# Kernel tuning notes

Hardware: AMD Instinct MI355X
Metric: run time of the kernel (lower is better)

## Reference

```python
import jax, jax.numpy as jnp
import numpy as np

GROUP_SIZE = 128  # per-group absmax scaling along the feature dim
ALPHA = 1.0       # group_size > 0 branch forces alpha = 1.0
# 4-bit signed non-uniform 'flint' grid (e2m1-style), sorted ascending, 15 levels
GRID_VALUES = np.array([-6.0, -4.0, -3.0, -2.0, -1.5, -1.0, -0.5, 0.0,
                        0.5, 1.0, 1.5, 2.0, 3.0, 4.0, 6.0], dtype=np.float32)


def quantize_with_grid(x, grid, group_size, alpha):
    """Group-wise fake quantization: scale each group by alpha*absmax/max|grid|,
    snap to nearest grid value, dequantize. Matches ANT quantize_with_grid."""
    orig_shape = x.shape
    xg = x.reshape(-1, group_size)                       # [G, group_size]
    gmax = jnp.max(jnp.abs(grid))
    maxv = jnp.max(jnp.abs(xg), axis=1, keepdims=True) * alpha
    scale = maxv / gmax                                  # [G, 1]
    scale = jnp.where(scale == 0, jnp.float32(1.0), scale)
    xs = xg / scale
    # nearest-grid lookup via midpoints + searchsorted (memory-light, exact)
    mid = (grid[1:] + grid[:-1]) * 0.5                   # [K-1]
    idx = jnp.searchsorted(mid, xs)                      # [G, group_size]
    q = jnp.take(grid, idx)
    return (q * scale).reshape(orig_shape)


def setup_inputs() -> dict:
    key = jax.random.key(0)
    k1, k2, k3 = jax.random.split(key, 3)
    x = jax.random.normal(k1, (4, 4096, 4096), dtype=jnp.float32)
    # weight buffer is the already-dequantized (calibrated) weight
    weight = jax.random.normal(k2, (1024, 4096), dtype=jnp.float32) * 0.02
    bias = jax.random.normal(k3, (1024,), dtype=jnp.float32) * 0.01
    grid = jnp.asarray(GRID_VALUES)
    return {"x": x, "weight": weight, "bias": bias, "grid": grid}


def reference(x, weight, bias, grid):
    # ANT_Linear.forward, calibrated steady state:
    #   input_2d = x.reshape(-1, in_features)
    #   deq_input = quantize_with_grid(input_2d, grid, group_size, alpha=1.0)
    #   out = F.linear(deq_input, weight) + bias
    out_shape = x.shape[:-1] + (weight.shape[0],)
    x2d = x.reshape(-1, x.shape[-1])                     # [N, in_features]
    deq = quantize_with_grid(x2d, grid, GROUP_SIZE, ALPHA)
    out = jnp.einsum('ni,oi->no', deq, weight) + bias    # [N, out_features]
    return out.reshape(out_shape)
```

## Files before the change

### kernel.cpp

```cpp
#include <hip/hip_runtime.h>
#include <hip/hip_bf16.h>

using bf16x8 = __attribute__((ext_vector_type(8))) __bf16;
using f32x4  = __attribute__((ext_vector_type(4))) float;
typedef unsigned short ushort_t;

#define M_DIM 16384
#define K_DIM 4096
#define N_DIM 1024

#define BARR() __builtin_amdgcn_s_barrier()

__device__ __forceinline__ unsigned short f2bf(float f) {
  __hip_bfloat16 h = __float2bfloat16(f);
  return *reinterpret_cast<unsigned short*>(&h);
}

__device__ __forceinline__ float snap(float a) {
  float q = 0.0f;
  q += (a > 0.25f) ? 0.5f : 0.0f;
  q += (a > 0.75f) ? 0.5f : 0.0f;
  q += (a > 1.25f) ? 0.5f : 0.0f;
  q += (a > 1.75f) ? 0.5f : 0.0f;
  q += (a > 2.5f)  ? 1.0f : 0.0f;
  q += (a > 3.5f)  ? 1.0f : 0.0f;
  q += (a > 5.0f)  ? 2.0f : 0.0f;
  return q;
}

__device__ __forceinline__ unsigned short qdq(float xv, float rs, float scale) {
  float xs = xv * rs;
  float q  = copysignf(snap(fabsf(xs)), xs);
  return f2bf(q * scale);
}

__global__ __launch_bounds__(256) void quant_kernel(const float* __restrict__ x,
                                                    unsigned short* __restrict__ dq) {
  const int wid = (blockIdx.x << 2) + (threadIdx.x >> 6);
  const int l   = threadIdx.x & 63;
  const int sub = l >> 4, t = l & 15;
  const size_t base = ((size_t)wid * 4 + sub) * 128;
  const float4* px = reinterpret_cast<const float4*>(x + base);
  float4 v0 = px[t];
  float4 v1 = px[16 + t];
  float amax = fmaxf(fmaxf(fmaxf(fabsf(v0.x), fabsf(v0.y)), fmaxf(fabsf(v0.z), fabsf(v0.w))),
                     fmaxf(fmaxf(fabsf(v1.x), fabsf(v1.y)), fmaxf(fabsf(v1.z), fabsf(v1.w))));
  #pragma unroll
  for (int m = 1; m < 16; m <<= 1) amax = fmaxf(amax, __shfl_xor(amax, m, 64));
  float scale = amax / 6.0f;
  if (scale == 0.0f) scale = 1.0f;
  const float rs = 1.0f / scale;
  ushort4 o0, o1;
  o0.x = qdq(v0.x, rs, scale); o0.y = qdq(v0.y, rs, scale);
  o0.z = qdq(v0.z, rs, scale); o0.w = qdq(v0.w, rs, scale);
  o1.x = qdq(v1.x, rs, scale); o1.y = qdq(v1.y, rs, scale);
  o1.z = qdq(v1.z, rs, scale); o1.w = qdq(v1.w, rs, scale);
  reinterpret_cast<ushort4*>(dq + base)[t]      = o0;
  reinterpret_cast<ushort4*>(dq + base)[16 + t] = o1;
}

__global__ __launch_bounds__(256) void wconv_kernel(const float* __restrict__ w,
                                                    unsigned short* __restrict__ o) {
  const int n4 = (N_DIM * K_DIM) / 4;
  for (int i = blockIdx.x * 256 + threadIdx.x; i < n4; i += gridDim.x * 256) {
    float4 v = reinterpret_cast<const float4*>(w)[i];
    ushort4 u;
    u.x = f2bf(v.x); u.y = f2bf(v.y); u.z = f2bf(v.z); u.w = f2bf(v.w);
    reinterpret_cast<ushort4*>(o)[i] = u;
  }
}

__device__ __forceinline__ bf16x8 lds_ld(const ushort_t* p) {
  return *reinterpret_cast<const bf16x8*>(p);
}

template<int OFF>
__device__ __forceinline__ void stg2(ushort_t (&sL)[65536], int wid,
                                     const ushort_t* g0, const ushort_t* g1) {
  __builtin_amdgcn_global_load_lds((const __attribute__((address_space(1))) void*)g0,
      (__attribute__((address_space(3))) void*)(&sL[OFF + wid * 512]), 16, 0, 0);
  __builtin_amdgcn_global_load_lds((const __attribute__((address_space(1))) void*)g1,
      (__attribute__((address_space(3))) void*)(&sL[OFF + 4096 + wid * 512]), 16, 0, 0);
}

template<int P, bool S12, bool S34, int VM>
__device__ __forceinline__ void tile_iter(
    int t, ushort_t (&sL)[65536], int wid, int rab, int rbb,
    const int (&roA)[8], const int (&roB)[4], int swz0, int swz1,
    const ushort_t* pa0, const ushort_t* pa1,
    const ushort_t* pb0, const ushort_t* pb1,
    f32x4 (&acc)[8][4]) {
  constexpr int RP  = P * 32768;
  constexpr int DB1 = (1 - P) * 32768 + 24576;
  constexpr int DA1 = (1 - P) * 32768 + 8192;
  constexpr int DB0 = P * 32768 + 16384;
  constexpr int DA0 = P * 32768;
  bf16x8 aL0[4], aL1[4], aH0[4], aH1[4], b0[4], b1[4];

  #pragma unroll
  for (int i = 0; i < 4; ++i) {
    aL0[i] = lds_ld(&sL[RP + rab + roA[i] + swz0]);
    aL1[i] = lds_ld(&sL[RP + rab + roA[i] + swz1]);
  }
  #pragma unroll
  for (int n = 0; n < 2; ++n) {
    b0[n] = lds_ld(&sL[RP + rbb + roB[n] + swz0]);
    b1[n] = lds_ld(&sL[RP + rbb + roB[n] + swz1]);
  }

  #pragma unroll
  for (int n = 2; n < 4; ++n) {
    b0[n] = lds_ld(&sL[RP + rbb + roB[n] + swz0]);
    b1[n] = lds_ld(&sL[RP + rbb + roB[n] + swz1]);
  }
  if constexpr (S12)
    stg2<DB1>(sL, wid, pb0 + (size_t)128 * K_DIM + (size_t)(t + 1) * 64,
                       pb1 + (size_t)128 * K_DIM + (size_t)(t + 1) * 64);
  __builtin_amdgcn_s_setprio(1);
  #pragma unroll
  for (int i = 0; i < 4; ++i)
    #pragma unroll
    for (int n = 0; n < 2; ++n) {
      acc[i][n] = __builtin_amdgcn_mfma_f32_16x16x32_bf16(aL0[i], b0[n], acc[i][n], 0, 0, 0);
      acc[i][n] = __builtin_amdgcn_mfma_f32_16x16x32_bf16(aL1[i], b1[n], acc[i][n], 0, 0, 0);
    }
  __builtin_amdgcn_s_setprio(0);
  BARR();

  #pragma unroll
  for (int i = 0; i < 4; ++i) {
    aH0[i] = lds_ld(&sL[RP + rab + roA[4 + i] + swz0]);
    aH1[i] = lds_ld(&sL[RP + rab + roA[4 + i] + swz1]);
  }
  if constexpr (S12)
    stg2<DA1>(sL, wid, pa0 + (size_t)128 * K_DIM + (size_t)(t + 1) * 64,
                       pa1 + (size_t)128 * K_DIM + (size_t)(t + 1) * 64);
  __builtin_amdgcn_s_setprio(1);
  #pragma unroll
  for (int i = 0; i < 4; ++i)
    #pragma unroll
    for (int n = 2; n < 4; ++n) {
      acc[i][n] = __builtin_amdgcn_mfma_f32_16x16x32_bf16(aL0[i], b0[n], acc[i][n], 0, 0, 0);
      acc[i][n] = __builtin_amdgcn_mfma_f32_16x16x32_bf16(aL1[i], b1[n], acc[i][n], 0, 0, 0);
    }
  __builtin_amdgcn_s_setprio(0);
  BARR();

  if constexpr (S34)
    stg2<DB0>(sL, wid, pb0 + (size_t)(t + 2) * 64, pb1 + (size_t)(t + 2) * 64);
  __builtin_amdgcn_s_setprio(1);
  #pragma unroll
  for (int i = 0; i < 4; ++i)
    #pragma unroll
    for (int n = 2; n < 4; ++n) {
      acc[4 + i][n] = __builtin_amdgcn_mfma_f32_16x16x32_bf16(aH0[i], b0[n], acc[4 + i][n], 0, 0, 0);
      acc[4 + i][n] = __builtin_amdgcn_mfma_f32_16x16x32_bf16(aH1[i], b1[n], acc[4 + i][n], 0, 0, 0);
    }
  __builtin_amdgcn_s_setprio(0);
  BARR();

  if constexpr (S34)
    stg2<DA0>(sL, wid, pa0 + (size_t)(t + 2) * 64, pa1 + (size_t)(t + 2) * 64);
  __builtin_amdgcn_s_setprio(1);
  #pragma unroll
  for (int i = 0; i < 4; ++i)
    #pragma unroll
    for (int n = 0; n < 2; ++n) {
      acc[4 + i][n] = __builtin_amdgcn_mfma_f32_16x16x32_bf16(aH0[i], b0[n], acc[4 + i][n], 0, 0, 0);
      acc[4 + i][n] = __builtin_amdgcn_mfma_f32_16x16x32_bf16(aH1[i], b1[n], acc[4 + i][n], 0, 0, 0);
    }
  __builtin_amdgcn_s_setprio(0);
  if constexpr (VM == 4) {
    asm volatile("s_waitcnt vmcnt(4)");
    __builtin_amdgcn_sched_barrier(0);
  } else if constexpr (VM == 0) {
    asm volatile("s_waitcnt vmcnt(0)");
    __builtin_amdgcn_sched_barrier(0);
  }
  BARR();
}

__global__ __launch_bounds__(512, 2) void gemm256(const ushort_t* __restrict__ A,
                                                  const ushort_t* __restrict__ B,
                                                  const float* __restrict__ bias,
                                                  float* __restrict__ C) {
  __shared__ ushort_t sL[65536];
  const int tid  = threadIdx.x;
  const int wid  = tid >> 6, lane = tid & 63;
  const int r    = lane & 15, h = lane >> 4;
  const int wm   = wid >> 2, wn = wid & 3;

  const int bid = blockIdx.x;
  const int xcd = bid & 7, j = bid >> 3;
  const int bm  = xcd * 8 + (j >> 2);
  const int bn  = j & 3;

  const int x7   = lane & 7;
  const int swz0 = ((h) ^ x7) << 3;
  const int swz1 = ((4 | h) ^ x7) << 3;
  int roA[8], roB[4];
  #pragma unroll
  for (int m = 0; m < 8; ++m) roA[m] = (m * 16 + r) * 64;
  #pragma unroll
  for (int n = 0; n < 4; ++n) roB[n] = ((wn & 1) * 64 + n * 16 + r) * 64;
  const int rab = wm * 8192;
  const int rbb = 16384 + (wn >> 1) * 8192;

  const int srow0 = tid >> 3;
  const int cst   = ((tid & 7) ^ (srow0 & 7)) << 3;
  const ushort_t* pa0 = A + (size_t)(bm * 256 + srow0) * K_DIM + cst;
  const ushort_t* pa1 = A + (size_t)(bm * 256 + 64 + srow0) * K_DIM + cst;
  const ushort_t* pb0 = B + (size_t)(bn * 256 + srow0) * K_DIM + cst;
  const ushort_t* pb1 = B + (size_t)(bn * 256 + 64 + srow0) * K_DIM + cst;

  f32x4 acc[8][4];
  #pragma unroll
  for (int m = 0; m < 8; ++m)
    #pragma unroll
    for (int n = 0; n < 4; ++n) acc[m][n] = (f32x4){0.f, 0.f, 0.f, 0.f};

  stg2<16384>(sL, wid, pb0, pb1);
  stg2<0>    (sL, wid, pa0, pa1);
  stg2<24576>(sL, wid, pb0 + (size_t)128 * K_DIM, pb1 + (size_t)128 * K_DIM);
  stg2<8192> (sL, wid, pa0 + (size_t)128 * K_DIM, pa1 + (size_t)128 * K_DIM);
  stg2<49152>(sL, wid, pb0 + 64, pb1 + 64);
  stg2<32768>(sL, wid, pa0 + 64, pa1 + 64);
  asm volatile("s_waitcnt vmcnt(4)");
  __builtin_amdgcn_sched_barrier(0);
  BARR();

  for (int t = 0; t < 62; t += 2) {
    tile_iter<0, true, true, 4>(t,     sL, wid, rab, rbb, roA, roB, swz0, swz1,
                                pa0, pa1, pb0, pb1, acc);
    tile_iter<1, true, true, 4>(t + 1, sL, wid, rab, rbb, roA, roB, swz0, swz1,
                                pa0, pa1, pb0, pb1, acc);
  }
  tile_iter<0, true, false, 0>(62, sL, wid, rab, rbb, roA, roB, swz0, swz1,
                               pa0, pa1, pb0, pb1, acc);
  tile_iter<1, false, false, -1>(63, sL, wid, rab, rbb, roA, roB, swz0, swz1,
                                 pa0, pa1, pb0, pb1, acc);

  const int orow = bm * 256 + wm * 128;
  const int ocol = bn * 256 + wn * 64;
  #pragma unroll
  for (int n = 0; n < 4; ++n) {
    const int col = ocol + n * 16 + r;
    const float bv = bias[col];
    #pragma unroll
    for (int m = 0; m < 8; ++m) {
      const int rb = orow + m * 16 + h * 4;
      #pragma unroll
      for (int j2 = 0; j2 < 4; ++j2)
        C[(size_t)(rb + j2) * N_DIM + col] = acc[m][n][j2] + bv;
    }
  }
}

__global__ __launch_bounds__(256) void fused_naive(const float* __restrict__ x,
                                                   const float* __restrict__ w,
                                                   const float* __restrict__ bias,
                                                   float* __restrict__ out) {
  __shared__ float xq[K_DIM];
  const int row = blockIdx.x;
  const float* xr = x + (size_t)row * K_DIM;
  const int t = threadIdx.x;
  const int g = t >> 3, s = t & 7;
  float vals[16];
  float amax = 0.f;
  #pragma unroll
  for (int i = 0; i < 16; ++i) {
    vals[i] = xr[g * 128 + s * 16 + i];
    amax = fmaxf(amax, fabsf(vals[i]));
  }
  #pragma unroll
  for (int m = 1; m < 8; m <<= 1) amax = fmaxf(amax, __shfl_xor(amax, m, 64));
  float scale = amax / 6.0f;
  if (scale == 0.f) scale = 1.f;
  const float rs = 1.0f / scale;
  #pragma unroll
  for (int i = 0; i < 16; ++i) {
    float xs = vals[i] * rs;
    xq[g * 128 + s * 16 + i] = copysignf(snap(fabsf(xs)), xs) * scale;
  }
  __syncthreads();
  #pragma unroll
  for (int i = 0; i < 4; ++i) {
    const int o = i * 256 + t;
    const float* wrow = w + (size_t)o * K_DIM;
    float acc = 0.f;
    for (int k = 0; k < K_DIM; k += 4) {
      float4 wv = *reinterpret_cast<const float4*>(wrow + k);
      acc += xq[k] * wv.x + xq[k + 1] * wv.y + xq[k + 2] * wv.z + xq[k + 3] * wv.w;
    }
    out[(size_t)row * N_DIM + o] = acc + bias[o];
  }
}

extern "C" void kernel_launch(void* const* d_in, const int* in_sizes, int n_in,
                              void* d_out, int out_size, void* d_ws, size_t ws_size,
                              hipStream_t stream) {
  const float* x    = (const float*)d_in[0];
  const float* wgt  = (const float*)d_in[1];
  const float* bias = (const float*)d_in[2];
  float* out = (float*)d_out;

  const size_t deq_bytes = (size_t)M_DIM * K_DIM * 2;
  const size_t wb_bytes  = (size_t)N_DIM * K_DIM * 2;
  if (ws_size >= deq_bytes + wb_bytes) {
    ushort_t* deq = (ushort_t*)d_ws;
    ushort_t* wb  = (ushort_t*)((char*)d_ws + deq_bytes);
    quant_kernel<<<(M_DIM * (K_DIM / 128)) / 16, 256, 0, stream>>>(x, deq);
    wconv_kernel<<<1024, 256, 0, stream>>>(wgt, wb);
    gemm256<<<(N_DIM / 256) * (M_DIM / 256), 512, 0, stream>>>(deq, wb, bias, out);
  } else {
    fused_naive<<<M_DIM, 256, 0, stream>>>(x, wgt, bias, out);
  }
}
```

Baseline: 191.0 us.

## Prefetch next tile's A-low and B-low LDS fragments across iteration boundary

The loads of the first A half and B half fragments for the next K tile move to the end of the current iteration, and those registers are carried across iterations. The vmcnt wait moves earlier with a tighter count so the next buffer is ready before the prefetch. The goal is to hide LDS read latency at the start of each tile behind the previous tile's MFMAs. In exchange, register pressure rises from the persistent fragments, and the altered wait placement could stall on global loads.

Result: slower. 358.9 us (+88.0%).

```diff
diff --git a/kernel.cpp b/kernel.cpp
--- a/kernel.cpp
+++ b/kernel.cpp
@@ -83,35 +83,27 @@
       (__attribute__((address_space(3))) void*)(&sL[OFF + 4096 + wid * 512]), 16, 0, 0);
 }
 
-template<int P, bool S12, bool S34, int VM>
+template<int P, bool S12, bool S34, int VM, bool PR>
 __device__ __forceinline__ void tile_iter(
     int t, ushort_t (&sL)[65536], int wid, int rab, int rbb,
     const int (&roA)[8], const int (&roB)[4], int swz0, int swz1,
     const ushort_t* pa0, const ushort_t* pa1,
     const ushort_t* pb0, const ushort_t* pb1,
+    bf16x8 (&aL0)[4], bf16x8 (&aL1)[4],
+    bf16x8 (&cb0)[2], bf16x8 (&cb1)[2],
     f32x4 (&acc)[8][4]) {
   constexpr int RP  = P * 32768;
-  constexpr int DB1 = (1 - P) * 32768 + 24576;
-  constexpr int DA1 = (1 - P) * 32768 + 8192;
-  constexpr int DB0 = P * 32768 + 16384;
-  constexpr int DA0 = P * 32768;
-  bf16x8 aL0[4], aL1[4], aH0[4], aH1[4], b0[4], b1[4];
-
-  #pragma unroll
-  for (int i = 0; i < 4; ++i) {
-    aL0[i] = lds_ld(&sL[RP + rab + roA[i] + swz0]);
-    aL1[i] = lds_ld(&sL[RP + rab + roA[i] + swz1]);
-  }
+  constexpr int NP  = (1 - P) * 32768;
+  constexpr int DB1 = NP + 24576;
+  constexpr int DA1 = NP + 8192;
+  constexpr int DB0 = RP + 16384;
+  constexpr int DA0 = RP;
+  bf16x8 aH0[4], aH1[4], bh0[2], bh1[2];
+
   #pragma unroll
   for (int n = 0; n < 2; ++n) {
-    b0[n] = lds_ld(&sL[RP + rbb + roB[n] + swz0]);
-    b1[n] = lds_ld(&sL[RP + rbb + roB[n] + swz1]);
-  }
-
-  #pragma unroll
-  for (int n = 2; n < 4; ++n) {
-    b0[n] = lds_ld(&sL[RP + rbb + roB[n] + swz0]);
-    b1[n] = lds_ld(&sL[RP + rbb + roB[n] + swz1]);
+    bh0[n] = lds_ld(&sL[RP + rbb + roB[2 + n] + swz0]);
+    bh1[n] = lds_ld(&sL[RP + rbb + roB[2 + n] + swz1]);
   }
   if constexpr (S12)
     stg2<DB1>(sL, wid, pb0 + (size_t)128 * K_DIM + (size_t)(t + 1) * 64,
@@ -121,8 +113,8 @@
   for (int i = 0; i < 4; ++i)
     #pragma unroll
     for (int n = 0; n < 2; ++n) {
-      acc[i][n] = __builtin_amdgcn_mfma_f32_16x16x32_bf16(aL0[i], b0[n], acc[i][n], 0, 0, 0);
-      acc[i][n] = __builtin_amdgcn_mfma_f32_16x16x32_bf16(aL1[i], b1[n], acc[i][n], 0, 0, 0);
+      acc[i][n] = __builtin_amdgcn_mfma_f32_16x16x32_bf16(aL0[i], cb0[n], acc[i][n], 0, 0, 0);
+      acc[i][n] = __builtin_amdgcn_mfma_f32_16x16x32_bf16(aL1[i], cb1[n], acc[i][n], 0, 0, 0);
     }
   __builtin_amdgcn_s_setprio(0);
   BARR();
@@ -139,9 +131,9 @@
   #pragma unroll
   for (int i = 0; i < 4; ++i)
     #pragma unroll
-    for (int n = 2; n < 4; ++n) {
-      acc[i][n] = __builtin_amdgcn_mfma_f32_16x16x32_bf16(aL0[i], b0[n], acc[i][n], 0, 0, 0);
-      acc[i][n] = __builtin_amdgcn_mfma_f32_16x16x32_bf16(aL1[i], b1[n], acc[i][n], 0, 0, 0);
+    for (int n = 0; n < 2; ++n) {
+      acc[i][2 + n] = __builtin_amdgcn_mfma_f32_16x16x32_bf16(aL0[i], bh0[n], acc[i][2 + n], 0, 0, 0);
+      acc[i][2 + n] = __builtin_amdgcn_mfma_f32_16x16x32_bf16(aL1[i], bh1[n], acc[i][2 + n], 0, 0, 0);
     }
   __builtin_amdgcn_s_setprio(0);
   BARR();
@@ -152,30 +144,42 @@
   #pragma unroll
   for (int i = 0; i < 4; ++i)
     #pragma unroll
-    for (int n = 2; n < 4; ++n) {
-      acc[4 + i][n] = __builtin_amdgcn_mfma_f32_16x16x32_bf16(aH0[i], b0[n], acc[4 + i][n], 0, 0, 0);
-      acc[4 + i][n] = __builtin_amdgcn_mfma_f32_16x16x32_bf16(aH1[i], b1[n], acc[4 + i][n], 0, 0, 0);
+    for (int n = 0; n < 2; ++n) {
+      acc[4 + i][2 + n] = __builtin_amdgcn_mfma_f32_16x16x32_bf16(aH0[i], bh0[n], acc[4 + i][2 + n], 0, 0, 0);
+      acc[4 + i][2 + n] = __builtin_amdgcn_mfma_f32_16x16x32_bf16(aH1[i], bh1[n], acc[4 + i][2 + n], 0, 0, 0);
     }
   __builtin_amdgcn_s_setprio(0);
-  BARR();
-
-  if constexpr (S34)
-    stg2<DA0>(sL, wid, pa0 + (size_t)(t + 2) * 64, pa1 + (size_t)(t + 2) * 64);
-  __builtin_amdgcn_s_setprio(1);
-  #pragma unroll
-  for (int i = 0; i < 4; ++i)
-    #pragma unroll
-    for (int n = 0; n < 2; ++n) {
-      acc[4 + i][n] = __builtin_amdgcn_mfma_f32_16x16x32_bf16(aH0[i], b0[n], acc[4 + i][n], 0, 0, 0);
-      acc[4 + i][n] = __builtin_amdgcn_mfma_f32_16x16x32_bf16(aH1[i], b1[n], acc[4 + i][n], 0, 0, 0);
-    }
-  __builtin_amdgcn_s_setprio(0);
-  if constexpr (VM == 4) {
-    asm volatile("s_waitcnt vmcnt(4)");
+  if constexpr (VM == 2) {
+    asm volatile("s_waitcnt vmcnt(2)");
     __builtin_amdgcn_sched_barrier(0);
   } else if constexpr (VM == 0) {
     asm volatile("s_waitcnt vmcnt(0)");
     __builtin_amdgcn_sched_barrier(0);
+  }
+  BARR();
+
+  if constexpr (S34)
+    stg2<DA0>(sL, wid, pa0 + (size_t)(t + 2) * 64, pa1 + (size_t)(t + 2) * 64);
+  __builtin_amdgcn_s_setprio(1);
+  #pragma unroll
+  for (int i = 0; i < 4; ++i)
+    #pragma unroll
+    for (int n = 0; n < 2; ++n) {
+      acc[4 + i][n] = __builtin_amdgcn_mfma_f32_16x16x32_bf16(aH0[i], cb0[n], acc[4 + i][n], 0, 0, 0);
+      acc[4 + i][n] = __builtin_amdgcn_mfma_f32_16x16x32_bf16(aH1[i], cb1[n], acc[4 + i][n], 0, 0, 0);
+    }
+  __builtin_amdgcn_s_setprio(0);
+  if constexpr (PR) {
+    #pragma unroll
+    for (int i = 0; i < 4; ++i) {
+      aL0[i] = lds_ld(&sL[NP + rab + roA[i] + swz0]);
+      aL1[i] = lds_ld(&sL[NP + rab + roA[i] + swz1]);
+    }
+    #pragma unroll
+    for (int n = 0; n < 2; ++n) {
+      cb0[n] = lds_ld(&sL[NP + rbb + roB[n] + swz0]);
+      cb1[n] = lds_ld(&sL[NP + rbb + roB[n] + swz1]);
+    }
   }
   BARR();
 }
@@ -229,16 +233,28 @@
   __builtin_amdgcn_sched_barrier(0);
   BARR();
 
+  bf16x8 aL0[4], aL1[4], cb0[2], cb1[2];
+  #pragma unroll
+  for (int i = 0; i < 4; ++i) {
+    aL0[i] = lds_ld(&sL[rab + roA[i] + swz0]);
+    aL1[i] = lds_ld(&sL[rab + roA[i] + swz1]);
+  }
+  #pragma unroll
+  for (int n = 0; n < 2; ++n) {
+    cb0[n] = lds_ld(&sL[rbb + roB[n] + swz0]);
+    cb1[n] = lds_ld(&sL[rbb + roB[n] + swz1]);
+  }
+
   for (int t = 0; t < 62; t += 2) {
-    tile_iter<0, true, true, 4>(t,     sL, wid, rab, rbb, roA, roB, swz0, swz1,
-                                pa0, pa1, pb0, pb1, acc);
-    tile_iter<1, true, true, 4>(t + 1, sL, wid, rab, rbb, roA, roB, swz0, swz1,
-                                pa0, pa1, pb0, pb1, acc);
-  }
-  tile_iter<0, true, false, 0>(62, sL, wid, rab, rbb, roA, roB, swz0, swz1,
-                               pa0, pa1, pb0, pb1, acc);
-  tile_iter<1, false, false, -1>(63, sL, wid, rab, rbb, roA, roB, swz0, swz1,
-                                 pa0, pa1, pb0, pb1, acc);
+    tile_iter<0, true, true, 2, true>(t,     sL, wid, rab, rbb, roA, roB, swz0, swz1,
+                                      pa0, pa1, pb0, pb1, aL0, aL1, cb0, cb1, acc);
+    tile_iter<1, true, true, 2, true>(t + 1, sL, wid, rab, rbb, roA, roB, swz0, swz1,
+                                      pa0, pa1, pb0, pb1, aL0, aL1, cb0, cb1, acc);
+  }
+  tile_iter<0, true, false, 0, true>(62, sL, wid, rab, rbb, roA, roB, swz0, swz1,
+                                     pa0, pa1, pb0, pb1, aL0, aL1, cb0, cb1, acc);
+  tile_iter<1, false, false, -1, false>(63, sL, wid, rab, rbb, roA, roB, swz0, swz1,
+                                        pa0, pa1, pb0, pb1, aL0, aL1, cb0, cb1, acc);
 
   const int orow = bm * 256 + wm * 128;
   const int ocol = bn * 256 + wn * 64;
```

## Load B fragments directly from global memory, halving LDS usage

Applied to the files above, without the earlier changes.

The B (weight) operand now goes straight from global memory into registers in the MFMA fragment layout, so it is no longer staged through shared memory. Shared memory shrinks to A only, and the vmcnt waits and prefetch offsets are adjusted to match. The aim is to cut LDS traffic and footprint. The cost is uncoalesced 16-byte global loads for B, duplicated across the wave rows that share B, and global latency exposed on the MFMA critical path with no prefetch of B.

New measurement: 292.0 us. 52.9% more time.

```diff
diff --git a/kernel.cpp b/kernel.cpp
--- a/kernel.cpp
+++ b/kernel.cpp
@@ -73,9 +73,12 @@
 __device__ __forceinline__ bf16x8 lds_ld(const ushort_t* p) {
   return *reinterpret_cast<const bf16x8*>(p);
 }
+__device__ __forceinline__ bf16x8 g_ld(const ushort_t* p) {
+  return *reinterpret_cast<const bf16x8*>(p);
+}
 
 template<int OFF>
-__device__ __forceinline__ void stg2(ushort_t (&sL)[65536], int wid,
+__device__ __forceinline__ void stg2(ushort_t (&sL)[32768], int wid,
                                      const ushort_t* g0, const ushort_t* g1) {
   __builtin_amdgcn_global_load_lds((const __attribute__((address_space(1))) void*)g0,
       (__attribute__((address_space(3))) void*)(&sL[OFF + wid * 512]), 16, 0, 0);
@@ -85,37 +88,27 @@
 
 template<int P, bool S12, bool S34, int VM>
 __device__ __forceinline__ void tile_iter(
-    int t, ushort_t (&sL)[65536], int wid, int rab, int rbb,
-    const int (&roA)[8], const int (&roB)[4], int swz0, int swz1,
+    int t, ushort_t (&sL)[32768], int wid, int rab,
+    const int (&roA)[8], int swz0, int swz1,
     const ushort_t* pa0, const ushort_t* pa1,
-    const ushort_t* pb0, const ushort_t* pb1,
+    const ushort_t* (&pB)[4],
     f32x4 (&acc)[8][4]) {
-  constexpr int RP  = P * 32768;
-  constexpr int DB1 = (1 - P) * 32768 + 24576;
-  constexpr int DA1 = (1 - P) * 32768 + 8192;
-  constexpr int DB0 = P * 32768 + 16384;
-  constexpr int DA0 = P * 32768;
+  constexpr int RP  = P * 16384;
+  constexpr int DA1 = (1 - P) * 16384 + 8192;
+  constexpr int DA0 = P * 16384;
   bf16x8 aL0[4], aL1[4], aH0[4], aH1[4], b0[4], b1[4];
 
+  #pragma unroll
+  for (int n = 0; n < 4; ++n) {
+    b0[n] = g_ld(pB[n]);
+    b1[n] = g_ld(pB[n] + 32);
+  }
   #pragma unroll
   for (int i = 0; i < 4; ++i) {
     aL0[i] = lds_ld(&sL[RP + rab + roA[i] + swz0]);
     aL1[i] = lds_ld(&sL[RP + rab + roA[i] + swz1]);
   }
-  #pragma unroll
-  for (int n = 0; n < 2; ++n) {
-    b0[n] = lds_ld(&sL[RP + rbb + roB[n] + swz0]);
-    b1[n] = lds_ld(&sL[RP + rbb + roB[n] + swz1]);
-  }
-
-  #pragma unroll
-  for (int n = 2; n < 4; ++n) {
-    b0[n] = lds_ld(&sL[RP + rbb + roB[n] + swz0]);
-    b1[n] = lds_ld(&sL[RP + rbb + roB[n] + swz1]);
-  }
-  if constexpr (S12)
-    stg2<DB1>(sL, wid, pb0 + (size_t)128 * K_DIM + (size_t)(t + 1) * 64,
-                       pb1 + (size_t)128 * K_DIM + (size_t)(t + 1) * 64);
+
   __builtin_amdgcn_s_setprio(1);
   #pragma unroll
   for (int i = 0; i < 4; ++i)
@@ -146,8 +139,6 @@
   __builtin_amdgcn_s_setprio(0);
   BARR();
 
-  if constexpr (S34)
-    stg2<DB0>(sL, wid, pb0 + (size_t)(t + 2) * 64, pb1 + (size_t)(t + 2) * 64);
   __builtin_amdgcn_s_setprio(1);
   #pragma unroll
   for (int i = 0; i < 4; ++i)
@@ -170,21 +161,24 @@
       acc[4 + i][n] = __builtin_amdgcn_mfma_f32_16x16x32_bf16(aH1[i], b1[n], acc[4 + i][n], 0, 0, 0);
     }
   __builtin_amdgcn_s_setprio(0);
-  if constexpr (VM == 4) {
-    asm volatile("s_waitcnt vmcnt(4)");
+  if constexpr (VM == 2) {
+    asm volatile("s_waitcnt vmcnt(2)");
     __builtin_amdgcn_sched_barrier(0);
   } else if constexpr (VM == 0) {
     asm volatile("s_waitcnt vmcnt(0)");
     __builtin_amdgcn_sched_barrier(0);
   }
   BARR();
+
+  #pragma unroll
+  for (int n = 0; n < 4; ++n) pB[n] += 64;
 }
 
 __global__ __launch_bounds__(512, 2) void gemm256(const ushort_t* __restrict__ A,
                                                   const ushort_t* __restrict__ B,
                                                   const float* __restrict__ bias,
                                                   float* __restrict__ C) {
-  __shared__ ushort_t sL[65536];
+  __shared__ ushort_t sL[32768];
   const int tid  = threadIdx.x;
   const int wid  = tid >> 6, lane = tid & 63;
   const int r    = lane & 15, h = lane >> 4;
@@ -198,20 +192,20 @@
   const int x7   = lane & 7;
   const int swz0 = ((h) ^ x7) << 3;
   const int swz1 = ((4 | h) ^ x7) << 3;
-  int roA[8], roB[4];
+  int roA[8];
   #pragma unroll
   for (int m = 0; m < 8; ++m) roA[m] = (m * 16 + r) * 64;
-  #pragma unroll
-  for (int n = 0; n < 4; ++n) roB[n] = ((wn & 1) * 64 + n * 16 + r) * 64;
   const int rab = wm * 8192;
-  const int rbb = 16384 + (wn >> 1) * 8192;
 
   const int srow0 = tid >> 3;
   const int cst   = ((tid & 7) ^ (srow0 & 7)) << 3;
   const ushort_t* pa0 = A + (size_t)(bm * 256 + srow0) * K_DIM + cst;
   const ushort_t* pa1 = A + (size_t)(bm * 256 + 64 + srow0) * K_DIM + cst;
-  const ushort_t* pb0 = B + (size_t)(bn * 256 + srow0) * K_DIM + cst;
-  const ushort_t* pb1 = B + (size_t)(bn * 256 + 64 + srow0) * K_DIM + cst;
+
+  const ushort_t* pB[4];
+  #pragma unroll
+  for (int n = 0; n < 4; ++n)
+    pB[n] = B + (size_t)(bn * 256 + wn * 64 + n * 16 + r) * K_DIM + h * 8;
 
   f32x4 acc[8][4];
   #pragma unroll
@@ -219,26 +213,23 @@
     #pragma unroll
     for (int n = 0; n < 4; ++n) acc[m][n] = (f32x4){0.f, 0.f, 0.f, 0.f};
 
-  stg2<16384>(sL, wid, pb0, pb1);
   stg2<0>    (sL, wid, pa0, pa1);
-  stg2<24576>(sL, wid, pb0 + (size_t)128 * K_DIM, pb1 + (size_t)128 * K_DIM);
   stg2<8192> (sL, wid, pa0 + (size_t)128 * K_DIM, pa1 + (size_t)128 * K_DIM);
-  stg2<49152>(sL, wid, pb0 + 64, pb1 + 64);
-  stg2<32768>(sL, wid, pa0 + 64, pa1 + 64);
-  asm volatile("s_waitcnt vmcnt(4)");
+  stg2<16384>(sL, wid, pa0 + 64, pa1 + 64);
+  asm volatile("s_waitcnt vmcnt(2)");
   __builtin_amdgcn_sched_barrier(0);
   BARR();
 
   for (int t = 0; t < 62; t += 2) {
-    tile_iter<0, true, true, 4>(t,     sL, wid, rab, rbb, roA, roB, swz0, swz1,
-                                pa0, pa1, pb0, pb1, acc);
-    tile_iter<1, true, true, 4>(t + 1, sL, wid, rab, rbb, roA, roB, swz0, swz1,
-                                pa0, pa1, pb0, pb1, acc);
-  }
-  tile_iter<0, true, false, 0>(62, sL, wid, rab, rbb, roA, roB, swz0, swz1,
-                               pa0, pa1, pb0, pb1, acc);
-  tile_iter<1, false, false, -1>(63, sL, wid, rab, rbb, roA, roB, swz0, swz1,
-                                 pa0, pa1, pb0, pb1, acc);
+    tile_iter<0, true, true, 2>(t,     sL, wid, rab, roA, swz0, swz1,
+                                pa0, pa1, pB, acc);
+    tile_iter<1, true, true, 2>(t + 1, sL, wid, rab, roA, swz0, swz1,
+                                pa0, pa1, pB, acc);
+  }
+  tile_iter<0, true, false, 0>(62, sL, wid, rab, roA, swz0, swz1,
+                               pa0, pa1, pB, acc);
+  tile_iter<1, false, false, -1>(63, sL, wid, rab, roA, swz0, swz1,
+                                 pa0, pa1, pB, acc);
 
   const int orow = bm * 256 + wm * 128;
   const int ocol = bn * 256 + wn * 64;
```
